# Performance work log

Measured on AMD Instinct MI355X. Metric: run time of the kernel, lower is better.

The kernel has to match this reference:

```python
import jax, jax.numpy as jnp
import numpy as np

B, S, E, H = 2, 2048, 2048, 16
NOPE, ROPE, VD = 128, 64, 128
QH = NOPE + ROPE  # 192
LORA = 512
ROPE_THETA = 10000.0
EPS = 1e-6


def setup_inputs() -> dict:
    key = jax.random.key(0)
    ks = jax.random.split(key, 5)
    sd = lambda n: 1.0 / np.sqrt(n)
    return {
        "x": jax.random.normal(ks[0], (B, S, E), jnp.float32),
        "wq": jax.random.normal(ks[1], (E, H * QH), jnp.float32) * sd(E),
        "wkv_a": jax.random.normal(ks[2], (E, LORA + ROPE), jnp.float32) * sd(E),
        "wkv_b": jax.random.normal(ks[3], (LORA, H * (NOPE + VD)), jnp.float32) * sd(LORA),
        "wo": jax.random.normal(ks[4], (H * VD, E), jnp.float32) * sd(H * VD),
        "kv_norm_scale": jnp.ones((LORA,), jnp.float32),
    }


def _rope(xp, cos, sin):
    # xp: (..., s, d); cos/sin: (s, d//2)
    d2 = xp.shape[-1] // 2
    x1, x2 = xp[..., :d2], xp[..., d2:]
    return jnp.concatenate([x1 * cos - x2 * sin, x2 * cos + x1 * sin], axis=-1)


def reference(x, wq, wkv_a, wkv_b, wo, kv_norm_scale):
    b, s, _ = x.shape
    # queries: (b, H, s, QH), split into no-pe / pe slices
    q = (x @ wq).reshape(b, s, H, QH).transpose(0, 2, 1, 3)
    q_nope, q_pe = q[..., :NOPE], q[..., NOPE:]

    # low-rank KV latent projection
    kva = x @ wkv_a  # (b, s, LORA + ROPE)
    ckv, k_pe = kva[..., :LORA], kva[..., LORA:]
    ckv = ckv * jax.lax.rsqrt(jnp.mean(ckv * ckv, axis=-1, keepdims=True) + EPS)
    ckv = ckv * kv_norm_scale  # RMSNorm on latent
    kv = (ckv @ wkv_b).reshape(b, s, H, NOPE + VD).transpose(0, 2, 1, 3)
    k_nope, v = kv[..., :NOPE], kv[..., NOPE:]

    # partial RoPE on the rope slice only
    pos = jnp.arange(s, dtype=jnp.float32)
    inv = 1.0 / (ROPE_THETA ** (jnp.arange(0, ROPE, 2, dtype=jnp.float32) / ROPE))
    ang = pos[:, None] * inv  # (s, ROPE//2)
    cos, sin = jnp.cos(ang), jnp.sin(ang)
    q_pe = _rope(q_pe, cos, sin)                 # (b, H, s, ROPE)
    k_pe = _rope(k_pe[:, None, :, :], cos, sin)  # (b, 1, s, ROPE), shared over heads

    # concat (the new_empty + slice-write in torch)
    qs = jnp.concatenate([q_nope, q_pe], axis=-1)  # (b, H, s, QH)
    ks_ = jnp.concatenate(
        [k_nope, jnp.broadcast_to(k_pe, (b, H, s, ROPE))], axis=-1
    )  # (b, H, s, QH)

    # causal SDPA with scale = q_head_dim**-0.5; asymmetric V head dim
    scale = QH ** -0.5
    scores = jnp.einsum('bhqd,bhkd->bhqk', qs, ks_) * scale
    causal = jnp.tril(jnp.ones((s, s), dtype=bool))
    scores = jnp.where(causal, scores, jnp.finfo(scores.dtype).min)
    attn = jax.nn.softmax(scores, axis=-1)
    out = jnp.einsum('bhqk,bhkd->bhqd', attn, v)  # (b, H, s, VD)
    out = out.transpose(0, 2, 1, 3).reshape(b, s, H * VD)
    return out @ wo
```

## Files before the change

kernel.cpp:

```cpp
#include <hip/hip_runtime.h>
#include <stdint.h>
#include <stddef.h>

typedef __bf16 bf16x8 __attribute__((ext_vector_type(8)));
typedef float floatx4 __attribute__((ext_vector_type(4)));
typedef unsigned short u16;

__device__ __forceinline__ float bf2f(u16 h) {
    unsigned u = ((unsigned)h) << 16;
    return __builtin_bit_cast(float, u);
}
__device__ __forceinline__ u16 f2bf(float f) {
    unsigned u = __builtin_bit_cast(unsigned, f);
    u += 0x7fffu + ((u >> 16) & 1u);
    return (u16)(u >> 16);
}

__device__ __forceinline__ void gload16(const void* g, void* l) {
    __builtin_amdgcn_global_load_lds(
        (const __attribute__((address_space(1))) uint32_t*)g,
        (__attribute__((address_space(3))) uint32_t*)l, 16, 0, 0);
}

__device__ __forceinline__ void wait_vm8() { asm volatile("s_waitcnt vmcnt(8)" ::: "memory"); }
__device__ __forceinline__ void wait_vm6() { asm volatile("s_waitcnt vmcnt(6)" ::: "memory"); }
__device__ __forceinline__ void wait_vm4() { asm volatile("s_waitcnt vmcnt(4)" ::: "memory"); }
__device__ __forceinline__ void wait_vm3() { asm volatile("s_waitcnt vmcnt(3)" ::: "memory"); }
__device__ __forceinline__ void wait_vm0() { asm volatile("s_waitcnt vmcnt(0)" ::: "memory"); }

__global__ __launch_bounds__(256) void k_conv_x(const float* __restrict__ in,
                                                u16* __restrict__ out, int n8) {
    int i = blockIdx.x * 256 + threadIdx.x;
    if (i >= n8) return;
    const float* f = in + (size_t)i * 8;
    unsigned o[4];
    for (int t = 0; t < 4; t++) {
        u16 lo = f2bf(f[2 * t]), hi = f2bf(f[2 * t + 1]);
        o[t] = (unsigned)lo | ((unsigned)hi << 16);
    }
    uint4 p = {o[0], o[1], o[2], o[3]};
    *(uint4*)&out[(size_t)i * 8] = p;
}

__global__ __launch_bounds__(256) void k_convT(const float* __restrict__ in,
                                               u16* __restrict__ out, int K, int N) {
    __shared__ u16 t[32][33];
    int k0 = blockIdx.x * 32, n0 = blockIdx.y * 32;
    int c = threadIdx.x & 31, r8 = threadIdx.x >> 5;
    for (int j = 0; j < 4; j++) {
        int row = r8 + j * 8;
        int n = n0 + c;
        t[row][c] = (n < N) ? f2bf(in[(size_t)(k0 + row) * N + n]) : (u16)0;
    }
    __syncthreads();
    for (int j = 0; j < 4; j++) {
        int row = r8 + j * 8;
        out[(size_t)(n0 + row) * K + k0 + c] = t[c][row];
    }
}

template <int NWC, int MODE>
__global__ __launch_bounds__(512, 2) void k_gemm256(const u16* __restrict__ A,
                                                    const u16* __restrict__ BT,
                                                    void* __restrict__ C0,
                                                    void* __restrict__ C1,
                                                    int K, int ldc) {
    constexpr int MFR = 16 / (8 / NWC);
    constexpr int ACH = 2;
    constexpr int BCH = NWC / 2;
    constexpr int SLOT = 8192 + NWC * 2048;
    __shared__ __align__(16) u16 RING[4][SLOT];
    int tid = threadIdx.x;
    int w = tid >> 6, lane = tid & 63;
    int l15 = lane & 15, quad = lane >> 4;
    int wr = w / NWC, wc = w % NWC;

    int gx = gridDim.x;
    int nwg = gx * gridDim.y;
    int flat = blockIdx.y * gx + blockIdx.x;
    int cpx = nwg >> 3;
    int swz = (flat & 7) * cpx + (flat >> 3);
    int bx = swz % gx, by = swz / gx;
    size_t m0 = (size_t)bx * 256, n0 = (size_t)by * (NWC * 64);
    int NT = K >> 5;

    const u16* srcA[ACH];
    const u16* srcB[BCH];
    int ldsAb[ACH], ldsBb[BCH];
#pragma unroll
    for (int p = 0; p < ACH; p++) {
        int chunk = p * 512 + tid;
        int s = chunk >> 6;
        int b = (chunk & 63) * 8;
        int bu = b ^ (((b >> 8) & 1) << 4);
        int r = bu >> 5, c = bu & 31;
        srcA[p] = A + (m0 + s * 16 + r) * (size_t)K + c;
        ldsAb[p] = (p * 512 + w * 64) * 8;
    }
#pragma unroll
    for (int p = 0; p < BCH; p++) {
        int chunk = p * 512 + tid;
        int s = chunk >> 6;
        int b = (chunk & 63) * 8;
        int bu = b ^ (((b >> 8) & 1) << 4);
        int r = bu >> 5, c = bu & 31;
        srcB[p] = BT + (n0 + s * 16 + r) * (size_t)K + c;
        ldsBb[p] = 8192 + (p * 512 + w * 64) * 8;
    }

    const int swb = (l15 * 32 + quad * 8) ^ ((l15 >> 3) << 4);

    floatx4 acc[MFR][4];
    const floatx4 fzero = {0.f, 0.f, 0.f, 0.f};
#pragma unroll
    for (int i = 0; i < MFR; i++)
#pragma unroll
        for (int j = 0; j < 4; j++) acc[i][j] = fzero;

    bf16x8 aA0[MFR], bB0[4], aA1[MFR], bB1[4];

    auto STAGE = [&](int j) {
        int rs = j & 3;
        size_t ko = (size_t)j * 32;
        u16* ring = &RING[rs][0];
#pragma unroll
        for (int p = 0; p < ACH; p++) gload16(srcA[p] + ko, ring + ldsAb[p]);
#pragma unroll
        for (int p = 0; p < BCH; p++) gload16(srcB[p] + ko, ring + ldsBb[p]);
    };
    auto READ0 = [&](int rs) {
        const u16* ring = &RING[rs][0];
#pragma unroll
        for (int i2 = 0; i2 < MFR; i2++)
            aA0[i2] = *(const bf16x8*)&ring[(wr * MFR + i2) * 512 + swb];
#pragma unroll
        for (int j2 = 0; j2 < 4; j2++)
            bB0[j2] = *(const bf16x8*)&ring[8192 + (wc * 4 + j2) * 512 + swb];
    };
    auto READ1 = [&](int rs) {
        const u16* ring = &RING[rs][0];
#pragma unroll
        for (int i2 = 0; i2 < MFR; i2++)
            aA1[i2] = *(const bf16x8*)&ring[(wr * MFR + i2) * 512 + swb];
#pragma unroll
        for (int j2 = 0; j2 < 4; j2++)
            bB1[j2] = *(const bf16x8*)&ring[8192 + (wc * 4 + j2) * 512 + swb];
    };
    auto MMA0 = [&]() {
#pragma unroll
        for (int i2 = 0; i2 < MFR; i2++)
#pragma unroll
            for (int j2 = 0; j2 < 4; j2++)
                acc[i2][j2] = __builtin_amdgcn_mfma_f32_16x16x32_bf16(
                    aA0[i2], bB0[j2], acc[i2][j2], 0, 0, 0);
    };
    auto MMA1 = [&]() {
#pragma unroll
        for (int i2 = 0; i2 < MFR; i2++)
#pragma unroll
            for (int j2 = 0; j2 < 4; j2++)
                acc[i2][j2] = __builtin_amdgcn_mfma_f32_16x16x32_bf16(
                    aA1[i2], bB1[j2], acc[i2][j2], 0, 0, 0);
    };

    STAGE(0); STAGE(1); STAGE(2);
    if constexpr (NWC == 4) wait_vm8(); else wait_vm6();
    __builtin_amdgcn_s_barrier();
    __builtin_amdgcn_sched_barrier(0);
    READ0(0);

    for (int j = 0; j + 1 < NT; j += 2) {
        if (j + 2 < NT) { if constexpr (NWC == 4) wait_vm4(); else wait_vm3(); }
        else wait_vm0();
        __builtin_amdgcn_s_barrier();
        __builtin_amdgcn_sched_barrier(0);
        READ1((j + 1) & 3);
        if (j + 3 < NT) STAGE(j + 3);
        MMA0();
        if (j + 2 < NT) {
            if (j + 3 < NT) { if constexpr (NWC == 4) wait_vm4(); else wait_vm3(); }
            else wait_vm0();
            __builtin_amdgcn_s_barrier();
            __builtin_amdgcn_sched_barrier(0);
            READ0((j + 2) & 3);
            if (j + 4 < NT) STAGE(j + 4);
        }
        MMA1();
    }

#pragma unroll
    for (int i = 0; i < MFR; i++)
#pragma unroll
        for (int j2 = 0; j2 < 4; j2++) {
            size_t col = n0 + wc * 64 + j2 * 16 + l15;
#pragma unroll
            for (int r = 0; r < 4; r++) {
                size_t row = m0 + (size_t)wr * (MFR * 16) + i * 16 + quad * 4 + r;
                if constexpr (MODE == 0) {
                    ((u16*)C0)[row * ldc + col] = f2bf(acc[i][j2][r]);
                } else if constexpr (MODE == 1) {
                    ((float*)C0)[row * ldc + col] = acc[i][j2][r];
                } else if constexpr (MODE == 2) {
                    if (col < 3072)
                        ((u16*)C0)[row * 3072 + col] = f2bf(acc[i][j2][r]);
                    else if (col < 3648)
                        ((u16*)C1)[row * 576 + (col - 3072)] = f2bf(acc[i][j2][r]);
                }
            }
            if constexpr (MODE == 3) {
                int cm = (int)(col & 255);
                size_t row0 = m0 + (size_t)wr * (MFR * 16) + i * 16 + quad * 4;
                if (cm < 128) {
#pragma unroll
                    for (int r = 0; r < 4; r++)
                        ((u16*)C0)[(row0 + r) * 4096 + col] = f2bf(acc[i][j2][r]);
                } else {
                    int h = (int)(col >> 8), vd = cm - 128;
                    size_t b = row0 >> 11, s = row0 & 2047;
                    unsigned lo = (unsigned)f2bf(acc[i][j2][0]) | ((unsigned)f2bf(acc[i][j2][1]) << 16);
                    unsigned hi = (unsigned)f2bf(acc[i][j2][2]) | ((unsigned)f2bf(acc[i][j2][3]) << 16);
                    uint2 pk = {lo, hi};
                    *(uint2*)&((u16*)C1)[(((b << 4) + h) * 128 + vd) * 2048 + s] = pk;
                }
            }
        }
}

__global__ __launch_bounds__(64) void k_rmsnorm(const u16* __restrict__ kva,
                                                const float* __restrict__ scl,
                                                u16* __restrict__ ckv) {
    int r = blockIdx.x, lane = threadIdx.x;
    const u16* row = kva + (size_t)r * 576 + lane * 8;
    uint4 raw = *(const uint4*)row;
    unsigned w[4] = {raw.x, raw.y, raw.z, raw.w};
    float f[8];
    float ss = 0.f;
    for (int t = 0; t < 4; t++) {
        f[2 * t]     = bf2f((u16)(w[t] & 0xffffu));
        f[2 * t + 1] = bf2f((u16)(w[t] >> 16));
        ss += f[2 * t] * f[2 * t] + f[2 * t + 1] * f[2 * t + 1];
    }
    for (int off = 1; off < 64; off <<= 1) ss += __shfl_xor(ss, off, 64);
    float rs = rsqrtf(ss * (1.f / 512.f) + 1e-6f);
    unsigned o[4];
    for (int t = 0; t < 4; t++) {
        u16 lo = f2bf(f[2 * t] * rs * scl[lane * 8 + 2 * t]);
        u16 hi = f2bf(f[2 * t + 1] * rs * scl[lane * 8 + 2 * t + 1]);
        o[t] = (unsigned)lo | ((unsigned)hi << 16);
    }
    uint4 packed = {o[0], o[1], o[2], o[3]};
    *(uint4*)(ckv + (size_t)r * 512 + lane * 8) = packed;
}

__global__ __launch_bounds__(256) void k_rope(u16* __restrict__ qbuf, u16* __restrict__ kva) {
    int tid = threadIdx.x;
    int rloc = tid >> 7;
    int task = tid & 127;
    int r = blockIdx.x * 2 + rloc;
    __shared__ float cs_s[2][32], sn_s[2][32];
    if (tid < 64) {
        int rr = tid >> 5, i = tid & 31;
        int ss = (blockIdx.x * 2 + rr) & 2047;
        float freq = __expf(-0.28782313662425575f * (float)i);
        float ang = (float)ss * freq;
        float sn, cs;
        sincosf(ang, &sn, &cs);
        cs_s[rr][i] = cs; sn_s[rr][i] = sn;
    }
    __syncthreads();
    if (task < 68) {
        int rb = task >> 2, q = task & 3;
        u16* base = (rb < 16) ? qbuf + (size_t)r * 3072 + rb * 192 + 128
                              : kva + (size_t)r * 576 + 512;
        u16* p1 = base + q * 8;
        uint4 x1v = *(uint4*)p1;
        uint4 x2v = *(uint4*)(p1 + 32);
        unsigned w1[4] = {x1v.x, x1v.y, x1v.z, x1v.w};
        unsigned w2[4] = {x2v.x, x2v.y, x2v.z, x2v.w};
        unsigned o1[4], o2[4];
        for (int t2 = 0; t2 < 4; t2++) {
            float a1 = bf2f((u16)(w1[t2] & 0xffffu)), b1 = bf2f((u16)(w1[t2] >> 16));
            float a2 = bf2f((u16)(w2[t2] & 0xffffu)), b2 = bf2f((u16)(w2[t2] >> 16));
            int i0 = q * 8 + t2 * 2, i1 = i0 + 1;
            float c0 = cs_s[rloc][i0], s0 = sn_s[rloc][i0];
            float c1 = cs_s[rloc][i1], s1 = sn_s[rloc][i1];
            o1[t2] = (unsigned)f2bf(a1 * c0 - a2 * s0) | ((unsigned)f2bf(b1 * c1 - b2 * s1) << 16);
            o2[t2] = (unsigned)f2bf(a2 * c0 + a1 * s0) | ((unsigned)f2bf(b2 * c1 + b1 * s1) << 16);
        }
        uint4 y1 = {o1[0], o1[1], o1[2], o1[3]};
        uint4 y2 = {o2[0], o2[1], o2[2], o2[3]};
        *(uint4*)p1 = y1;
        *(uint4*)(p1 + 32) = y2;
    }
}

__global__ __launch_bounds__(256, 3) void k_attn(const u16* __restrict__ qbuf,
                                                 const u16* __restrict__ kv,
                                                 const u16* __restrict__ kva,
                                                 const u16* __restrict__ vt,
                                                 u16* __restrict__ attno) {
    int tid = threadIdx.x;
    int wave = tid >> 6, lane = tid & 63;
    int quad = lane >> 4, l15 = lane & 15;
    int hb = blockIdx.x;
    int h = hb & 15, b = hb >> 4;
    int qb = 31 - (int)blockIdx.y;
    int qg0 = qb * 64 + wave * 16;
    int row = qg0 + l15;

    __shared__ __align__(16) u16 Kn[2][32 * 136];
    __shared__ __align__(16) u16 Kp[2][32 * 72];
    __shared__ __align__(16) u16 Vs[2][128 * 40];
    __shared__ __align__(16) u16 P[4][16 * 40];

    const u16* qrp = qbuf + ((size_t)(b * 2048) + qg0 + l15) * 3072 + h * 192;
    bf16x8 qf[6];
    for (int c = 0; c < 6; c++) qf[c] = *(const bf16x8*)&qrp[c * 32 + quad * 8];

    const floatx4 fzero = {0.f, 0.f, 0.f, 0.f};
    floatx4 o[8];
    for (int f = 0; f < 8; f++) o[f] = fzero;
    float lp = 0.f;

    const u16* kvb = kv  + (size_t)(b * 2048) * 4096 + h * 256;
    const u16* kpb = kva + (size_t)(b * 2048) * 576 + 512;
    const u16* vtb = vt  + (size_t)(b * 16 + h) * 128 * 2048;
    const float scale = 0.07216878364870323f;

    int nkt = qb * 2 + 2;

    int kKey0 = tid >> 4,          kOff0 = (tid & 15) * 8;
    int kKey1 = (tid + 256) >> 4,  kOff1 = (tid & 15) * 8;
    int pKey  = tid >> 3,          pOff  = (tid & 7) * 8;
    int vRow0 = tid >> 2,          vOff0 = (tid & 3) * 8;
    int vRow1 = (tid + 256) >> 2,  vOff1 = (tid & 3) * 8;

    {
        uint4 a = *(const uint4*)&kvb[(size_t)kKey0 * 4096 + kOff0];
        uint4 c = *(const uint4*)&kvb[(size_t)kKey1 * 4096 + kOff1];
        uint4 d = *(const uint4*)&kpb[(size_t)pKey * 576 + pOff];
        uint4 e = *(const uint4*)&vtb[(size_t)vRow0 * 2048 + vOff0];
        uint4 g = *(const uint4*)&vtb[(size_t)vRow1 * 2048 + vOff1];
        *(uint4*)&Kn[0][kKey0 * 136 + kOff0] = a;
        *(uint4*)&Kn[0][kKey1 * 136 + kOff1] = c;
        *(uint4*)&Kp[0][pKey * 72 + pOff] = d;
        *(uint4*)&Vs[0][vRow0 * 40 + vOff0] = e;
        *(uint4*)&Vs[0][vRow1 * 40 + vOff1] = g;
    }
    __syncthreads();

    for (int kt = 0; kt < nkt; kt++) {
        int cur = kt & 1;
        bool have = (kt + 1) < nkt;
        uint4 sA = {}, sB = {}, sC = {}, sD = {}, sE = {};
        if (have) {
            int kb = (kt + 1) * 32;
            sA = *(const uint4*)&kvb[(size_t)(kb + kKey0) * 4096 + kOff0];
            sB = *(const uint4*)&kvb[(size_t)(kb + kKey1) * 4096 + kOff1];
            sC = *(const uint4*)&kpb[(size_t)(kb + pKey) * 576 + pOff];
            sD = *(const uint4*)&vtb[(size_t)vRow0 * 2048 + kb + vOff0];
            sE = *(const uint4*)&vtb[(size_t)vRow1 * 2048 + kb + vOff1];
        }
        if (kt * 32 <= qg0 + 15) {
            bf16x8 vf[8];
            for (int f = 0; f < 8; f++)
                vf[f] = *(const bf16x8*)&Vs[cur][(f * 16 + l15) * 40 + quad * 8];
            floatx4 sc[2] = {fzero, fzero};
            for (int hf = 0; hf < 2; hf++) {
                const u16* kn = &Kn[cur][(hf * 16 + l15) * 136];
                const u16* kp = &Kp[cur][(hf * 16 + l15) * 72];
                for (int c = 0; c < 4; c++) {
                    bf16x8 kf = *(const bf16x8*)&kn[c * 32 + quad * 8];
                    sc[hf] = __builtin_amdgcn_mfma_f32_16x16x32_bf16(kf, qf[c], sc[hf], 0, 0, 0);
                }
                for (int c = 0; c < 2; c++) {
                    bf16x8 kf = *(const bf16x8*)&kp[c * 32 + quad * 8];
                    sc[hf] = __builtin_amdgcn_mfma_f32_16x16x32_bf16(kf, qf[4 + c], sc[hf], 0, 0, 0);
                }
            }
            asm volatile("" ::: "memory");
            for (int hf = 0; hf < 2; hf++) {
                int keyb = kt * 32 + hf * 16 + quad * 4;
                float p[4];
                for (int r = 0; r < 4; r++)
                    p[r] = (keyb + r <= row) ? __expf(sc[hf][r] * scale) : 0.f;
                lp += (p[0] + p[1]) + (p[2] + p[3]);
                unsigned d0 = (unsigned)f2bf(p[0]) | ((unsigned)f2bf(p[1]) << 16);
                unsigned d1 = (unsigned)f2bf(p[2]) | ((unsigned)f2bf(p[3]) << 16);
                uint2 pk = {d0, d1};
                *(uint2*)&P[wave][l15 * 40 + hf * 16 + quad * 4] = pk;
            }
            asm volatile("" ::: "memory");
            bf16x8 pa = *(const bf16x8*)&P[wave][l15 * 40 + quad * 8];
            asm volatile("" ::: "memory");
            for (int f = 0; f < 8; f++)
                o[f] = __builtin_amdgcn_mfma_f32_16x16x32_bf16(pa, vf[f], o[f], 0, 0, 0);
        }
        if (have) {
            int nb = cur ^ 1;
            *(uint4*)&Kn[nb][kKey0 * 136 + kOff0] = sA;
            *(uint4*)&Kn[nb][kKey1 * 136 + kOff1] = sB;
            *(uint4*)&Kp[nb][pKey * 72 + pOff] = sC;
            *(uint4*)&Vs[nb][vRow0 * 40 + vOff0] = sD;
            *(uint4*)&Vs[nb][vRow1 * 40 + vOff1] = sE;
        }
        __syncthreads();
    }

    lp += __shfl_xor(lp, 16, 64);
    lp += __shfl_xor(lp, 32, 64);
    float lrow[4];
    for (int r = 0; r < 4; r++) lrow[r] = __shfl(lp, quad * 4 + r, 64);
    for (int f = 0; f < 8; f++)
        for (int r = 0; r < 4; r++) {
            int orow = qg0 + quad * 4 + r;
            float val = o[f][r] / lrow[r];
            attno[((size_t)(b * 2048) + orow) * 2048 + h * 128 + f * 16 + l15] = f2bf(val);
        }
}

extern "C" void kernel_launch(void* const* d_in, const int* in_sizes, int n_in,
                              void* d_out, int out_size, void* d_ws, size_t ws_size,
                              hipStream_t stream) {
    const float* x_raw    = (const float*)d_in[0];
    const float* wq_raw   = (const float*)d_in[1];
    const float* wkva_raw = (const float*)d_in[2];
    const float* wkvb_raw = (const float*)d_in[3];
    const float* wo_raw   = (const float*)d_in[4];
    const float* kvs_raw  = (const float*)d_in[5];
    float* out = (float*)d_out;
    u16* ws = (u16*)d_ws;

    const size_t O_ATT = 0;
    const size_t O_VT  = 8388608;
    const size_t O_QB  = 16777216;
    const size_t O_KVA = 29360128;
    const size_t O_KV  = 31719424;
    const size_t TOTAL_BYTES = 48496640ull * 2;
    if (ws_size < TOTAL_BYTES) return;

    u16* g12bt  = ws + O_ATT;
    u16* ckv    = ws + O_ATT;
    u16* wkvb_t = ws + O_ATT + 2097152;
    u16* attno  = ws + O_ATT;
    u16* x_bf   = ws + O_VT;
    u16* vt     = ws + O_VT;
    u16* qbuf   = ws + O_QB;
    u16* wo_t   = ws + O_QB;
    u16* kva    = ws + O_KVA;
    u16* kv     = ws + O_KV;

    k_conv_x<<<4096, 256, 0, stream>>>(x_raw, x_bf, 1048576);
    k_convT<<<dim3(64, 96), 256, 0, stream>>>(wq_raw, g12bt, 2048, 3072);
    k_convT<<<dim3(64, 20), 256, 0, stream>>>(wkva_raw, g12bt + (size_t)3072 * 2048, 2048, 576);

    k_gemm256<2, 2><<<dim3(16, 29), 512, 0, stream>>>(x_bf, g12bt, qbuf, kva, 2048, 0);

    k_rmsnorm<<<4096, 64, 0, stream>>>(kva, kvs_raw, ckv);
    k_convT<<<dim3(16, 128), 256, 0, stream>>>(wkvb_raw, wkvb_t, 512, 4096);
    k_gemm256<2, 3><<<dim3(16, 32), 512, 0, stream>>>(ckv, wkvb_t, kv, vt, 512, 4096);

    k_rope<<<2048, 256, 0, stream>>>(qbuf, kva);

    k_attn<<<dim3(32, 32), 256, 0, stream>>>(qbuf, kv, kva, vt, attno);

    k_convT<<<dim3(64, 64), 256, 0, stream>>>(wo_raw, wo_t, 2048, 2048);
    k_gemm256<2, 1><<<dim3(16, 16), 512, 0, stream>>>(attno, wo_t, out, nullptr, 2048, 2048);
}
```

Baseline: 372.6 us.

## Merge preprocessing and norm/rope kernels and compact k_nope storage

Folds the x conversion and all four weight transpose-converts into one grid-partitioned preprocessing kernel, and merges RMSNorm and RoPE into one kernel, cutting the launch count. The kv-B GEMM epilogue now stores only k_nope with a 2048-wide row stride, since V already goes to a separate transposed buffer, and the attention kernel reads that compact layout. This halves that buffer's write traffic and tightens the attention K loads. The weight buffers move to the freed workspace region so every transpose can run up front, at the cost of more workspace use and branchy block dispatch.

```diff
diff --git a/kernel.cpp b/kernel.cpp
--- a/kernel.cpp
+++ b/kernel.cpp
@@ -22,31 +22,36 @@
         (__attribute__((address_space(3))) uint32_t*)l, 16, 0, 0);
 }
 
-__device__ __forceinline__ void wait_vm8() { asm volatile("s_waitcnt vmcnt(8)" ::: "memory"); }
 __device__ __forceinline__ void wait_vm6() { asm volatile("s_waitcnt vmcnt(6)" ::: "memory"); }
-__device__ __forceinline__ void wait_vm4() { asm volatile("s_waitcnt vmcnt(4)" ::: "memory"); }
 __device__ __forceinline__ void wait_vm3() { asm volatile("s_waitcnt vmcnt(3)" ::: "memory"); }
 __device__ __forceinline__ void wait_vm0() { asm volatile("s_waitcnt vmcnt(0)" ::: "memory"); }
 
-__global__ __launch_bounds__(256) void k_conv_x(const float* __restrict__ in,
-                                                u16* __restrict__ out, int n8) {
-    int i = blockIdx.x * 256 + threadIdx.x;
-    if (i >= n8) return;
-    const float* f = in + (size_t)i * 8;
-    unsigned o[4];
-    for (int t = 0; t < 4; t++) {
-        u16 lo = f2bf(f[2 * t]), hi = f2bf(f[2 * t + 1]);
-        o[t] = (unsigned)lo | ((unsigned)hi << 16);
-    }
-    uint4 p = {o[0], o[1], o[2], o[3]};
-    *(uint4*)&out[(size_t)i * 8] = p;
-}
-
-__global__ __launch_bounds__(256) void k_convT(const float* __restrict__ in,
-                                               u16* __restrict__ out, int K, int N) {
+__global__ __launch_bounds__(256) void k_preproc(const float* __restrict__ x_raw, u16* __restrict__ x_bf,
+                                                 const float* __restrict__ wq, const float* __restrict__ wkva,
+                                                 const float* __restrict__ wkvb, const float* __restrict__ wo,
+                                                 u16* __restrict__ g12bt, u16* __restrict__ wkvb_t,
+                                                 u16* __restrict__ wo_t) {
     __shared__ u16 t[32][33];
-    int k0 = blockIdx.x * 32, n0 = blockIdx.y * 32;
-    int c = threadIdx.x & 31, r8 = threadIdx.x >> 5;
+    int bid = blockIdx.x, tid = threadIdx.x;
+    if (bid < 4096) {
+        int i = bid * 256 + tid;
+        const float* f = x_raw + (size_t)i * 8;
+        unsigned o[4];
+        for (int q = 0; q < 4; q++) {
+            u16 lo = f2bf(f[2 * q]), hi = f2bf(f[2 * q + 1]);
+            o[q] = (unsigned)lo | ((unsigned)hi << 16);
+        }
+        uint4 p = {o[0], o[1], o[2], o[3]};
+        *(uint4*)&x_bf[(size_t)i * 8] = p;
+        return;
+    }
+    const float* in; u16* out; int K, N, bx, by;
+    if (bid < 10240)      { int i = bid - 4096;  in = wq;   out = g12bt;                       K = 2048; N = 3072; bx = i & 63; by = i >> 6; }
+    else if (bid < 11520) { int i = bid - 10240; in = wkva; out = g12bt + (size_t)3072 * 2048; K = 2048; N = 576;  bx = i & 63; by = i >> 6; }
+    else if (bid < 13568) { int i = bid - 11520; in = wkvb; out = wkvb_t;                      K = 512;  N = 4096; bx = i & 15; by = i >> 4; }
+    else                  { int i = bid - 13568; in = wo;   out = wo_t;                        K = 2048; N = 2048; bx = i & 63; by = i >> 6; }
+    int k0 = bx * 32, n0 = by * 32;
+    int c = tid & 31, r8 = tid >> 5;
     for (int j = 0; j < 4; j++) {
         int row = r8 + j * 8;
         int n = n0 + c;
@@ -164,22 +169,20 @@
     };
 
     STAGE(0); STAGE(1); STAGE(2);
-    if constexpr (NWC == 4) wait_vm8(); else wait_vm6();
+    wait_vm6();
     __builtin_amdgcn_s_barrier();
     __builtin_amdgcn_sched_barrier(0);
     READ0(0);
 
     for (int j = 0; j + 1 < NT; j += 2) {
-        if (j + 2 < NT) { if constexpr (NWC == 4) wait_vm4(); else wait_vm3(); }
-        else wait_vm0();
+        if (j + 2 < NT) wait_vm3(); else wait_vm0();
         __builtin_amdgcn_s_barrier();
         __builtin_amdgcn_sched_barrier(0);
         READ1((j + 1) & 3);
         if (j + 3 < NT) STAGE(j + 3);
         MMA0();
         if (j + 2 < NT) {
-            if (j + 3 < NT) { if constexpr (NWC == 4) wait_vm4(); else wait_vm3(); }
-            else wait_vm0();
+            if (j + 3 < NT) wait_vm3(); else wait_vm0();
             __builtin_amdgcn_s_barrier();
             __builtin_amdgcn_sched_barrier(0);
             READ0((j + 2) & 3);
@@ -211,9 +214,10 @@
                 int cm = (int)(col & 255);
                 size_t row0 = m0 + (size_t)wr * (MFR * 16) + i * 16 + quad * 4;
                 if (cm < 128) {
+                    size_t cc = (col >> 8) * 128 + cm;
 #pragma unroll
                     for (int r = 0; r < 4; r++)
-                        ((u16*)C0)[(row0 + r) * 4096 + col] = f2bf(acc[i][j2][r]);
+                        ((u16*)C0)[(row0 + r) * 2048 + cc] = f2bf(acc[i][j2][r]);
                 } else {
                     int h = (int)(col >> 8), vd = cm - 128;
                     size_t b = row0 >> 11, s = row0 & 2047;
@@ -226,41 +230,44 @@
         }
 }
 
-__global__ __launch_bounds__(64) void k_rmsnorm(const u16* __restrict__ kva,
-                                                const float* __restrict__ scl,
-                                                u16* __restrict__ ckv) {
-    int r = blockIdx.x, lane = threadIdx.x;
-    const u16* row = kva + (size_t)r * 576 + lane * 8;
-    uint4 raw = *(const uint4*)row;
-    unsigned w[4] = {raw.x, raw.y, raw.z, raw.w};
-    float f[8];
-    float ss = 0.f;
-    for (int t = 0; t < 4; t++) {
-        f[2 * t]     = bf2f((u16)(w[t] & 0xffffu));
-        f[2 * t + 1] = bf2f((u16)(w[t] >> 16));
-        ss += f[2 * t] * f[2 * t] + f[2 * t + 1] * f[2 * t + 1];
-    }
-    for (int off = 1; off < 64; off <<= 1) ss += __shfl_xor(ss, off, 64);
-    float rs = rsqrtf(ss * (1.f / 512.f) + 1e-6f);
-    unsigned o[4];
-    for (int t = 0; t < 4; t++) {
-        u16 lo = f2bf(f[2 * t] * rs * scl[lane * 8 + 2 * t]);
-        u16 hi = f2bf(f[2 * t + 1] * rs * scl[lane * 8 + 2 * t + 1]);
-        o[t] = (unsigned)lo | ((unsigned)hi << 16);
-    }
-    uint4 packed = {o[0], o[1], o[2], o[3]};
-    *(uint4*)(ckv + (size_t)r * 512 + lane * 8) = packed;
-}
-
-__global__ __launch_bounds__(256) void k_rope(u16* __restrict__ qbuf, u16* __restrict__ kva) {
-    int tid = threadIdx.x;
+__global__ __launch_bounds__(256) void k_normrope(const u16* __restrict__ kva_c,
+                                                  const float* __restrict__ scl,
+                                                  u16* __restrict__ ckv,
+                                                  u16* __restrict__ qbuf,
+                                                  u16* __restrict__ kva) {
+    __shared__ float cs_s[2][32], sn_s[2][32];
+    int bid = blockIdx.x, tid = threadIdx.x;
+    if (bid < 1024) {
+        int r = bid * 4 + (tid >> 6), lane = tid & 63;
+        const u16* row = kva_c + (size_t)r * 576 + lane * 8;
+        uint4 raw = *(const uint4*)row;
+        unsigned w[4] = {raw.x, raw.y, raw.z, raw.w};
+        float f[8];
+        float ss = 0.f;
+        for (int t = 0; t < 4; t++) {
+            f[2 * t]     = bf2f((u16)(w[t] & 0xffffu));
+            f[2 * t + 1] = bf2f((u16)(w[t] >> 16));
+            ss += f[2 * t] * f[2 * t] + f[2 * t + 1] * f[2 * t + 1];
+        }
+        for (int off = 1; off < 64; off <<= 1) ss += __shfl_xor(ss, off, 64);
+        float rs = rsqrtf(ss * (1.f / 512.f) + 1e-6f);
+        unsigned o[4];
+        for (int t = 0; t < 4; t++) {
+            u16 lo = f2bf(f[2 * t] * rs * scl[lane * 8 + 2 * t]);
+            u16 hi = f2bf(f[2 * t + 1] * rs * scl[lane * 8 + 2 * t + 1]);
+            o[t] = (unsigned)lo | ((unsigned)hi << 16);
+        }
+        uint4 packed = {o[0], o[1], o[2], o[3]};
+        *(uint4*)(ckv + (size_t)r * 512 + lane * 8) = packed;
+        return;
+    }
+    int rb2 = bid - 1024;
     int rloc = tid >> 7;
     int task = tid & 127;
-    int r = blockIdx.x * 2 + rloc;
-    __shared__ float cs_s[2][32], sn_s[2][32];
+    int r = rb2 * 2 + rloc;
     if (tid < 64) {
         int rr = tid >> 5, i = tid & 31;
-        int ss = (blockIdx.x * 2 + rr) & 2047;
+        int ss = (rb2 * 2 + rr) & 2047;
         float freq = __expf(-0.28782313662425575f * (float)i);
         float ang = (float)ss * freq;
         float sn, cs;
@@ -322,7 +329,7 @@
     for (int f = 0; f < 8; f++) o[f] = fzero;
     float lp = 0.f;
 
-    const u16* kvb = kv  + (size_t)(b * 2048) * 4096 + h * 256;
+    const u16* kvb = kv  + (size_t)(b * 2048) * 2048 + h * 128;
     const u16* kpb = kva + (size_t)(b * 2048) * 576 + 512;
     const u16* vtb = vt  + (size_t)(b * 16 + h) * 128 * 2048;
     const float scale = 0.07216878364870323f;
@@ -336,8 +343,8 @@
     int vRow1 = (tid + 256) >> 2,  vOff1 = (tid & 3) * 8;
 
     {
-        uint4 a = *(const uint4*)&kvb[(size_t)kKey0 * 4096 + kOff0];
-        uint4 c = *(const uint4*)&kvb[(size_t)kKey1 * 4096 + kOff1];
+        uint4 a = *(const uint4*)&kvb[(size_t)kKey0 * 2048 + kOff0];
+        uint4 c = *(const uint4*)&kvb[(size_t)kKey1 * 2048 + kOff1];
         uint4 d = *(const uint4*)&kpb[(size_t)pKey * 576 + pOff];
         uint4 e = *(const uint4*)&vtb[(size_t)vRow0 * 2048 + vOff0];
         uint4 g = *(const uint4*)&vtb[(size_t)vRow1 * 2048 + vOff1];
@@ -355,8 +362,8 @@
         uint4 sA = {}, sB = {}, sC = {}, sD = {}, sE = {};
         if (have) {
             int kb = (kt + 1) * 32;
-            sA = *(const uint4*)&kvb[(size_t)(kb + kKey0) * 4096 + kOff0];
-            sB = *(const uint4*)&kvb[(size_t)(kb + kKey1) * 4096 + kOff1];
+            sA = *(const uint4*)&kvb[(size_t)(kb + kKey0) * 2048 + kOff0];
+            sB = *(const uint4*)&kvb[(size_t)(kb + kKey1) * 2048 + kOff1];
             sC = *(const uint4*)&kpb[(size_t)(kb + pKey) * 576 + pOff];
             sD = *(const uint4*)&vtb[(size_t)vRow0 * 2048 + kb + vOff0];
             sE = *(const uint4*)&vtb[(size_t)vRow1 * 2048 + kb + vOff1];
@@ -436,34 +443,32 @@
     const size_t O_QB  = 16777216;
     const size_t O_KVA = 29360128;
     const size_t O_KV  = 31719424;
+    const size_t O_WOT = O_KV + 8388608;
+    const size_t O_WBT = O_WOT + 4194304;
     const size_t TOTAL_BYTES = 48496640ull * 2;
     if (ws_size < TOTAL_BYTES) return;
 
     u16* g12bt  = ws + O_ATT;
     u16* ckv    = ws + O_ATT;
-    u16* wkvb_t = ws + O_ATT + 2097152;
     u16* attno  = ws + O_ATT;
     u16* x_bf   = ws + O_VT;
     u16* vt     = ws + O_VT;
     u16* qbuf   = ws + O_QB;
-    u16* wo_t   = ws + O_QB;
     u16* kva    = ws + O_KVA;
     u16* kv     = ws + O_KV;
-
-    k_conv_x<<<4096, 256, 0, stream>>>(x_raw, x_bf, 1048576);
-    k_convT<<<dim3(64, 96), 256, 0, stream>>>(wq_raw, g12bt, 2048, 3072);
-    k_convT<<<dim3(64, 20), 256, 0, stream>>>(wkva_raw, g12bt + (size_t)3072 * 2048, 2048, 576);
+    u16* wo_t   = ws + O_WOT;
+    u16* wkvb_t = ws + O_WBT;
+
+    k_preproc<<<17664, 256, 0, stream>>>(x_raw, x_bf, wq_raw, wkva_raw, wkvb_raw, wo_raw,
+                                         g12bt, wkvb_t, wo_t);
 
     k_gemm256<2, 2><<<dim3(16, 29), 512, 0, stream>>>(x_bf, g12bt, qbuf, kva, 2048, 0);
 
-    k_rmsnorm<<<4096, 64, 0, stream>>>(kva, kvs_raw, ckv);
-    k_convT<<<dim3(16, 128), 256, 0, stream>>>(wkvb_raw, wkvb_t, 512, 4096);
+    k_normrope<<<3072, 256, 0, stream>>>(kva, kvs_raw, ckv, qbuf, kva);
+
     k_gemm256<2, 3><<<dim3(16, 32), 512, 0, stream>>>(ckv, wkvb_t, kv, vt, 512, 4096);
 
-    k_rope<<<2048, 256, 0, stream>>>(qbuf, kva);
-
     k_attn<<<dim3(32, 32), 256, 0, stream>>>(qbuf, kv, kva, vt, attno);
 
-    k_convT<<<dim3(64, 64), 256, 0, stream>>>(wo_raw, wo_t, 2048, 2048);
     k_gemm256<2, 1><<<dim3(16, 16), 512, 0, stream>>>(attno, wo_t, out, nullptr, 2048, 2048);
 }
```

Measured after the change: 390.2 us. 4.7% more time.

## Use wider GEMM tiles with four-stage single-buffer pipeline for projections

Applied to the files above, without the earlier changes.

Switches the QKV-A and KV-B projection GEMMs to the NWC=4 variant, which doubles the tile width so half as many blocks are launched. The NWC=4 main loop is rewritten as a one-tile-per-iteration pipeline with three stages in flight and explicit drain steps. The wkv_a transpose grid grows to cover the padded columns the wider tile reads. Fewer, larger tiles improve operand reuse but cut the block count and may lower occupancy, and the new prologue and drain rely on exact vmcnt accounting.

```diff
diff --git a/kernel.cpp b/kernel.cpp
--- a/kernel.cpp
+++ b/kernel.cpp
@@ -164,28 +164,57 @@
     };
 
     STAGE(0); STAGE(1); STAGE(2);
-    if constexpr (NWC == 4) wait_vm8(); else wait_vm6();
-    __builtin_amdgcn_s_barrier();
-    __builtin_amdgcn_sched_barrier(0);
-    READ0(0);
-
-    for (int j = 0; j + 1 < NT; j += 2) {
-        if (j + 2 < NT) { if constexpr (NWC == 4) wait_vm4(); else wait_vm3(); }
-        else wait_vm0();
+
+    if constexpr (NWC == 4) {
+        int j = 0;
+        for (; j + 3 < NT; j++) {
+            wait_vm8();
+            __builtin_amdgcn_s_barrier();
+            __builtin_amdgcn_sched_barrier(0);
+            READ0(j & 3);
+            STAGE(j + 3);
+            __builtin_amdgcn_sched_barrier(0);
+            MMA0();
+        }
+        {
+            wait_vm8();
+            __builtin_amdgcn_s_barrier();
+            __builtin_amdgcn_sched_barrier(0);
+            READ0(j & 3); MMA0(); j++;
+        }
+        {
+            wait_vm4();
+            __builtin_amdgcn_s_barrier();
+            __builtin_amdgcn_sched_barrier(0);
+            READ0(j & 3); MMA0(); j++;
+        }
+        {
+            wait_vm0();
+            __builtin_amdgcn_s_barrier();
+            __builtin_amdgcn_sched_barrier(0);
+            READ0(j & 3); MMA0();
+        }
+    } else {
+        wait_vm6();
         __builtin_amdgcn_s_barrier();
         __builtin_amdgcn_sched_barrier(0);
-        READ1((j + 1) & 3);
-        if (j + 3 < NT) STAGE(j + 3);
-        MMA0();
-        if (j + 2 < NT) {
-            if (j + 3 < NT) { if constexpr (NWC == 4) wait_vm4(); else wait_vm3(); }
-            else wait_vm0();
+        READ0(0);
+        for (int j = 0; j + 1 < NT; j += 2) {
+            if (j + 2 < NT) wait_vm3(); else wait_vm0();
             __builtin_amdgcn_s_barrier();
             __builtin_amdgcn_sched_barrier(0);
-            READ0((j + 2) & 3);
-            if (j + 4 < NT) STAGE(j + 4);
-        }
-        MMA1();
+            READ1((j + 1) & 3);
+            if (j + 3 < NT) STAGE(j + 3);
+            MMA0();
+            if (j + 2 < NT) {
+                if (j + 3 < NT) wait_vm3(); else wait_vm0();
+                __builtin_amdgcn_s_barrier();
+                __builtin_amdgcn_sched_barrier(0);
+                READ0((j + 2) & 3);
+                if (j + 4 < NT) STAGE(j + 4);
+            }
+            MMA1();
+        }
     }
 
 #pragma unroll
@@ -452,13 +481,13 @@
 
     k_conv_x<<<4096, 256, 0, stream>>>(x_raw, x_bf, 1048576);
     k_convT<<<dim3(64, 96), 256, 0, stream>>>(wq_raw, g12bt, 2048, 3072);
-    k_convT<<<dim3(64, 20), 256, 0, stream>>>(wkva_raw, g12bt + (size_t)3072 * 2048, 2048, 576);
-
-    k_gemm256<2, 2><<<dim3(16, 29), 512, 0, stream>>>(x_bf, g12bt, qbuf, kva, 2048, 0);
+    k_convT<<<dim3(64, 24), 256, 0, stream>>>(wkva_raw, g12bt + (size_t)3072 * 2048, 2048, 576);
+
+    k_gemm256<4, 2><<<dim3(16, 15), 512, 0, stream>>>(x_bf, g12bt, qbuf, kva, 2048, 0);
 
     k_rmsnorm<<<4096, 64, 0, stream>>>(kva, kvs_raw, ckv);
     k_convT<<<dim3(16, 128), 256, 0, stream>>>(wkvb_raw, wkvb_t, 512, 4096);
-    k_gemm256<2, 3><<<dim3(16, 32), 512, 0, stream>>>(ckv, wkvb_t, kv, vt, 512, 4096);
+    k_gemm256<4, 3><<<dim3(16, 16), 512, 0, stream>>>(ckv, wkvb_t, kv, vt, 512, 4096);
 
     k_rope<<<2048, 256, 0, stream>>>(qbuf, kva);
 
```

Result: faster. 354.1 us (-4.9%).
